# Performance work log

Hardware: AMD Instinct MI355X
Metric: run time of the kernel (lower is better)

The kernel has to match this reference:

```python
import jax, jax.numpy as jnp
import numpy as np


def setup_inputs() -> dict:
    key = jax.random.key(0)
    ks = jax.random.split(key, 5)
    B, S, C = 512, 512, 96
    emissions = jax.random.normal(ks[0], (B, S, C), dtype=jnp.float32)
    tags = jax.random.randint(ks[1], (B, S), 0, C, dtype=jnp.int64)
    masks = jnp.ones((B, S), dtype=bool)
    start_transitions = jax.random.uniform(ks[2], (C,), jnp.float32, -0.1, 0.1)
    end_transitions = jax.random.uniform(ks[3], (C,), jnp.float32, -0.1, 0.1)
    transitions = jax.random.uniform(ks[4], (C, C), jnp.float32, -0.1, 0.1)
    return {
        "emissions": emissions,
        "tags": tags,
        "masks": masks,
        "start_transitions": start_transitions,
        "end_transitions": end_transitions,
        "transitions": transitions,
    }


def _crf_llh(emissions, tags, masks, start_transitions, end_transitions, transitions):
    # to time-major: (S, B, C), (S, B)
    emissions = jnp.swapaxes(emissions, 0, 1)
    tags = jnp.swapaxes(tags, 0, 1)
    masks = jnp.swapaxes(masks, 0, 1)
    S, B, C = emissions.shape
    maskf = masks.astype(emissions.dtype)

    # ---- numerator: score of the gold tag path (fully vectorized over time) ----
    em_scores = jnp.take_along_axis(emissions, tags[:, :, None], axis=2)[:, :, 0]  # (S, B)
    trans_scores = transitions[tags[:-1], tags[1:]]  # (S-1, B)
    score = start_transitions[tags[0]] + em_scores[0]
    score = score + jnp.sum((trans_scores + em_scores[1:]) * maskf[1:], axis=0)
    seq_ends = masks.astype(jnp.int32).sum(axis=0) - 1  # (B,)
    last_tags = tags[seq_ends, jnp.arange(B)]
    numerator = score + end_transitions[last_tags]

    # ---- denominator: forward algorithm (sequential logsumexp recurrence) ----
    alpha0 = start_transitions[None, :] + emissions[0]  # (B, C)

    def step(alpha, inp):
        em_i, m_i = inp  # (B, C), (B,)
        # (B, C_prev, C_next)
        scores = alpha[:, :, None] + transitions[None, :, :] + em_i[:, None, :]
        next_alpha = jax.scipy.special.logsumexp(scores, axis=1)
        alpha = jnp.where(m_i[:, None], next_alpha, alpha)
        return alpha, None

    alpha, _ = jax.lax.scan(step, alpha0, (emissions[1:], masks[1:]))
    denominator = jax.scipy.special.logsumexp(alpha + end_transitions[None, :], axis=1)

    return jnp.mean(numerator - denominator)


def reference(emissions, tags, masks, start_transitions, end_transitions, transitions):
    return _crf_llh(emissions, tags, masks, start_transitions, end_transitions, transitions)
```

## Files before the change

### kernel.cpp

```cpp
#include <hip/hip_runtime.h>
#include <hip/hip_bf16.h>
#include <math.h>


#define BATCH 512
#define SEQ   512
#define NC    96
#define NTHR  64
#define NEG_INF (-1e30f)
#define SC    0.25f
#define LSC   1.3862943611198906f

typedef __fp16 half2v __attribute__((ext_vector_type(2)));

#define DPP_STEP_F(v, op, ctrl)                                              \
    v = op(v, __int_as_float(__builtin_amdgcn_update_dpp(                    \
            __float_as_int(v), __float_as_int(v), (ctrl), 0xf, 0xf, false)))

__device__ __forceinline__ float wave_max_all(float v) {
    DPP_STEP_F(v, fmaxf, 0x111);
    DPP_STEP_F(v, fmaxf, 0x112);
    DPP_STEP_F(v, fmaxf, 0x114);
    DPP_STEP_F(v, fmaxf, 0x118);
    DPP_STEP_F(v, fmaxf, 0x142);
    DPP_STEP_F(v, fmaxf, 0x143);
    return __int_as_float(__builtin_amdgcn_readlane(__float_as_int(v), 63));
}
__device__ __forceinline__ float fadd_(float a, float b) { return a + b; }
__device__ __forceinline__ float wave_sum_all(float v) {
    DPP_STEP_F(v, fadd_, 0x111);
    DPP_STEP_F(v, fadd_, 0x112);
    DPP_STEP_F(v, fadd_, 0x114);
    DPP_STEP_F(v, fadd_, 0x118);
    DPP_STEP_F(v, fadd_, 0x142);
    DPP_STEP_F(v, fadd_, 0x143);
    return __int_as_float(__builtin_amdgcn_readlane(__float_as_int(v), 63));
}

__global__ __launch_bounds__(NTHR, 1)
void crf_llh_kernel(const float* __restrict__ em,
                    const int*   __restrict__ tags,
                    const int*   __restrict__ masks,
                    const float* __restrict__ startT,
                    const float* __restrict__ endT,
                    const float* __restrict__ trans,
                    float*       __restrict__ out)
{
    const int b = blockIdx.x;
    const int l = threadIdx.x;
    const bool active = (l < 48);
    const int j0 = active ? 2 * l     : 0;
    const int j1 = active ? 2 * l + 1 : 0;

    __shared__ __align__(16) half2v qsh[48];

    const float* em_b    = em    + (size_t)b * SEQ * NC;
    const int*   tags_b  = tags  + b * SEQ;
    const int*   masks_b = masks + b * SEQ;

    half2v e0[48], e1[48];
    #pragma unroll
    for (int k = 0; k < 48; ++k) {
        const float t00 = trans[(2 * k)     * NC + j0];
        const float t01 = trans[(2 * k + 1) * NC + j0];
        const float t10 = trans[(2 * k)     * NC + j1];
        const float t11 = trans[(2 * k + 1) * NC + j1];
        e0[k] = __builtin_amdgcn_cvt_pkrtz(__expf(t00), __expf(t01));
        e1[k] = __builtin_amdgcn_cvt_pkrtz(__expf(t10), __expf(t11));
    }

    float a0 = active ? (startT[j0] + em_b[j0]) : NEG_INF;
    float a1 = active ? (startT[j1] + em_b[j1]) : NEG_INF;
    float m  = wave_max_all(fmaxf(a0, a1));

    const float2* em2 = reinterpret_cast<const float2*>(em_b);
    float2 emA = em2[1 * (NC / 2) + l % 48];
    float2 emB = em2[2 * (NC / 2) + l % 48];
    int mkA = masks_b[1];
    int mkB = masks_b[2];

    for (int s = 1; s < SEQ; ++s) {
        const int sp = (s + 2 < SEQ) ? (s + 2) : (SEQ - 1);
        const float2 emN = em2[sp * (NC / 2) + l % 48];
        const int    mkN = masks_b[sp];

        const float wm = wave_max_all(fmaxf(a0, a1));

        const float p0 = __expf(a0 - m) * SC;
        const float p1 = __expf(a1 - m) * SC;
        const half2v ph = __builtin_amdgcn_cvt_pkrtz(p0, p1);
        if (active) qsh[l] = ph;
        __syncthreads();

        float acc0a = 0.f, acc0b = 0.f, acc1a = 0.f, acc1b = 0.f;
        const uint4* q4 = reinterpret_cast<const uint4*>(qsh);
        #pragma unroll
        for (int t = 0; t < 12; ++t) {
            const uint4 qv = q4[t];
            const half2v qx = __builtin_bit_cast(half2v, qv.x);
            const half2v qy = __builtin_bit_cast(half2v, qv.y);
            const half2v qz = __builtin_bit_cast(half2v, qv.z);
            const half2v qw = __builtin_bit_cast(half2v, qv.w);
            acc0a = __builtin_amdgcn_fdot2(qx, e0[4 * t + 0], acc0a, false);
            acc1a = __builtin_amdgcn_fdot2(qx, e1[4 * t + 0], acc1a, false);
            acc0a = __builtin_amdgcn_fdot2(qy, e0[4 * t + 1], acc0a, false);
            acc1a = __builtin_amdgcn_fdot2(qy, e1[4 * t + 1], acc1a, false);
            acc0b = __builtin_amdgcn_fdot2(qz, e0[4 * t + 2], acc0b, false);
            acc1b = __builtin_amdgcn_fdot2(qz, e1[4 * t + 2], acc1b, false);
            acc0b = __builtin_amdgcn_fdot2(qw, e0[4 * t + 3], acc0b, false);
            acc1b = __builtin_amdgcn_fdot2(qw, e1[4 * t + 3], acc1b, false);
        }
        const float acc0 = acc0a + acc0b;
        const float acc1 = acc1a + acc1b;

        const bool upd = active && (mkA != 0);
        const float na0 = m + __logf(acc0) + LSC + emA.x;
        const float na1 = m + __logf(acc1) + LSC + emA.y;
        a0 = upd ? na0 : a0;
        a1 = upd ? na1 : a1;
        m = wm;

        emA = emB; emB = emN;
        mkA = mkB; mkB = mkN;
    }

    const float v0 = active ? (a0 + endT[j0]) : NEG_INF;
    const float v1 = active ? (a1 + endT[j1]) : NEG_INF;
    const float M  = wave_max_all(fmaxf(v0, v1));
    const float e  = active ? (__expf(v0 - M) + __expf(v1 - M)) : 0.f;
    const float denom = M + __logf(wave_sum_all(e));

    float nsum = 0.f;
    float msum = 0.f;
    #pragma unroll
    for (int k = 0; k < SEQ / NTHR; ++k) {
        const int s  = l + NTHR * k;
        const int tg = tags_b[s];
        const int mk = masks_b[s];
        msum += (mk ? 1.f : 0.f);
        if (s == 0) {
            nsum += startT[tg] + em_b[tg];
        } else if (mk) {
            nsum += trans[tags_b[s - 1] * NC + tg] + em_b[s * NC + tg];
        }
    }
    nsum = wave_sum_all(nsum);
    msum = wave_sum_all(msum);
    if (l == 0) {
        const int cnt  = (int)msum;
        const int last = tags_b[cnt - 1];
        atomicAdd(out, (nsum + endT[last] - denom) * (1.0f / (float)BATCH));
    }
}

extern "C" void kernel_launch(void* const* d_in, const int* in_sizes, int n_in,
                              void* d_out, int out_size, void* d_ws, size_t ws_size,
                              hipStream_t stream) {
    const float* em     = (const float*)d_in[0];
    const int*   tags   = (const int*)  d_in[1];
    const int*   masks  = (const int*)  d_in[2];
    const float* startT = (const float*)d_in[3];
    const float* endT   = (const float*)d_in[4];
    const float* trans  = (const float*)d_in[5];
    float* out = (float*)d_out;

    (void)hipMemsetAsync(out, 0, sizeof(float), stream);
    crf_llh_kernel<<<BATCH, NTHR, 0, stream>>>(em, tags, masks, startT, endT, trans, out);
}
```

Baseline: 420.6 us.

## Batch 16 sequences per wave and compute forward recurrence with MFMA

The kernel now handles 16 batch rows per single-wave block and computes each step's 16x96 by 96x96 product of exp(alpha) and exp(transitions) with fp16 MFMA instead of per-lane dot products. Each row is rescaled by a power of two taken from its max exponent, and the exponents are accumulated in an integer, so no logs are needed inside the loop. The aim is to replace scalar fdot2 work and one block per sequence with matrix-core throughput. The cost is only 32 blocks on a large GPU, LDS round-trips each step, and added fp16 rounding error.

```diff
diff --git a/kernel.cpp b/kernel.cpp
--- a/kernel.cpp
+++ b/kernel.cpp
@@ -6,26 +6,20 @@
 #define BATCH 512
 #define SEQ   512
 #define NC    96
-#define NTHR  64
-#define NEG_INF (-1e30f)
-#define SC    0.25f
-#define LSC   1.3862943611198906f
+#define CH    16
+#define NBLK  (BATCH / CH)
+#define PAD   104
+#define LN2   0.69314718055994531f
+#define LN2X4 2.7725887222397812f
 
 typedef __fp16 half2v __attribute__((ext_vector_type(2)));
+typedef __fp16 half8v __attribute__((ext_vector_type(8)));
+typedef float  f32x4  __attribute__((ext_vector_type(4)));
 
 #define DPP_STEP_F(v, op, ctrl)                                              \
     v = op(v, __int_as_float(__builtin_amdgcn_update_dpp(                    \
             __float_as_int(v), __float_as_int(v), (ctrl), 0xf, 0xf, false)))
 
-__device__ __forceinline__ float wave_max_all(float v) {
-    DPP_STEP_F(v, fmaxf, 0x111);
-    DPP_STEP_F(v, fmaxf, 0x112);
-    DPP_STEP_F(v, fmaxf, 0x114);
-    DPP_STEP_F(v, fmaxf, 0x118);
-    DPP_STEP_F(v, fmaxf, 0x142);
-    DPP_STEP_F(v, fmaxf, 0x143);
-    return __int_as_float(__builtin_amdgcn_readlane(__float_as_int(v), 63));
-}
 __device__ __forceinline__ float fadd_(float a, float b) { return a + b; }
 __device__ __forceinline__ float wave_sum_all(float v) {
     DPP_STEP_F(v, fadd_, 0x111);
@@ -36,8 +30,15 @@
     DPP_STEP_F(v, fadd_, 0x143);
     return __int_as_float(__builtin_amdgcn_readlane(__float_as_int(v), 63));
 }
-
-__global__ __launch_bounds__(NTHR, 1)
+__device__ __forceinline__ float bperm_f(int lanesrc, float v) {
+    return __int_as_float(__builtin_amdgcn_ds_bpermute(
+        (lanesrc & 63) << 2, __float_as_int(v)));
+}
+__device__ __forceinline__ int bperm_i(int lanesrc, int v) {
+    return __builtin_amdgcn_ds_bpermute((lanesrc & 63) << 2, v);
+}
+
+__global__ __launch_bounds__(64, 1)
 void crf_llh_kernel(const float* __restrict__ em,
                     const int*   __restrict__ tags,
                     const int*   __restrict__ masks,
@@ -48,109 +49,188 @@
 {
     const int b = blockIdx.x;
     const int l = threadIdx.x;
-    const bool active = (l < 48);
-    const int j0 = active ? 2 * l     : 0;
-    const int j1 = active ? 2 * l + 1 : 0;
-
-    __shared__ __align__(16) half2v qsh[48];
-
-    const float* em_b    = em    + (size_t)b * SEQ * NC;
-    const int*   tags_b  = tags  + b * SEQ;
-    const int*   masks_b = masks + b * SEQ;
-
-    half2v e0[48], e1[48];
-    #pragma unroll
-    for (int k = 0; k < 48; ++k) {
-        const float t00 = trans[(2 * k)     * NC + j0];
-        const float t01 = trans[(2 * k + 1) * NC + j0];
-        const float t10 = trans[(2 * k)     * NC + j1];
-        const float t11 = trans[(2 * k + 1) * NC + j1];
-        e0[k] = __builtin_amdgcn_cvt_pkrtz(__expf(t00), __expf(t01));
-        e1[k] = __builtin_amdgcn_cvt_pkrtz(__expf(t10), __expf(t11));
-    }
-
-    float a0 = active ? (startT[j0] + em_b[j0]) : NEG_INF;
-    float a1 = active ? (startT[j1] + em_b[j1]) : NEG_INF;
-    float m  = wave_max_all(fmaxf(a0, a1));
-
-    const float2* em2 = reinterpret_cast<const float2*>(em_b);
-    float2 emA = em2[1 * (NC / 2) + l % 48];
-    float2 emB = em2[2 * (NC / 2) + l % 48];
-    int mkA = masks_b[1];
-    int mkB = masks_b[2];
+    const int c = l & 15;
+    const int q = l >> 4;
+
+    __shared__ __fp16 wl[CH * PAD];
+    __shared__ float  maxsh[CH];
+
+    half8v Bf[3][6];
+    #pragma unroll
+    for (int kt = 0; kt < 3; ++kt) {
+        #pragma unroll
+        for (int nt = 0; nt < 6; ++nt) {
+            #pragma unroll
+            for (int jp = 0; jp < 4; ++jp) {
+                const int k0 = 32 * kt + 8 * q + 2 * jp;
+                const int n  = 16 * nt + c;
+                const half2v pe = __builtin_amdgcn_cvt_pkrtz(
+                    __expf(trans[(k0)     * NC + n]),
+                    __expf(trans[(k0 + 1) * NC + n]));
+                Bf[kt][nt][2 * jp]     = pe[0];
+                Bf[kt][nt][2 * jp + 1] = pe[1];
+            }
+        }
+    }
+
+    const size_t gc = (size_t)(b * CH + c);
+    const float* em_c = em + gc * SEQ * NC;
+    const int*   mk_c = masks + gc * SEQ;
+    const int*   tg_c = tags  + gc * SEQ;
+
+    half8v Af[3];
+    float M0;
+    int   S;
+    {
+        float a0[24];
+        float mx = -1e30f;
+        #pragma unroll
+        for (int kt = 0; kt < 3; ++kt)
+            #pragma unroll
+            for (int j = 0; j < 8; ++j) {
+                const int k = 32 * kt + 8 * q + j;
+                const float v = startT[k] + em_c[k];
+                a0[kt * 8 + j] = v;
+                mx = fmaxf(mx, v);
+            }
+        mx = fmaxf(mx, bperm_f(l ^ 16, mx));
+        mx = fmaxf(mx, bperm_f(l ^ 32, mx));
+        M0 = mx;
+        S  = 1;
+        #pragma unroll
+        for (int kt = 0; kt < 3; ++kt)
+            #pragma unroll
+            for (int j = 0; j < 8; ++j)
+                Af[kt][j] = (__fp16)(__expf(a0[kt * 8 + j] - M0) * 0.5f);
+    }
+
+    size_t emb[4];
+    #pragma unroll
+    for (int r = 0; r < 4; ++r)
+        emb[r] = (size_t)(b * CH + 4 * q + r) * SEQ * NC + c;
+
+    float emA[24], emB[24];
+    #pragma unroll
+    for (int nt = 0; nt < 6; ++nt)
+        #pragma unroll
+        for (int r = 0; r < 4; ++r) {
+            emA[nt * 4 + r] = em[emb[r] + (size_t)1 * NC + 16 * nt];
+            emB[nt * 4 + r] = em[emb[r] + (size_t)2 * NC + 16 * nt];
+        }
+    int mkA = mk_c[1], mkB = mk_c[2];
 
     for (int s = 1; s < SEQ; ++s) {
         const int sp = (s + 2 < SEQ) ? (s + 2) : (SEQ - 1);
-        const float2 emN = em2[sp * (NC / 2) + l % 48];
-        const int    mkN = masks_b[sp];
-
-        const float wm = wave_max_all(fmaxf(a0, a1));
-
-        const float p0 = __expf(a0 - m) * SC;
-        const float p1 = __expf(a1 - m) * SC;
-        const half2v ph = __builtin_amdgcn_cvt_pkrtz(p0, p1);
-        if (active) qsh[l] = ph;
-        __syncthreads();
-
-        float acc0a = 0.f, acc0b = 0.f, acc1a = 0.f, acc1b = 0.f;
-        const uint4* q4 = reinterpret_cast<const uint4*>(qsh);
-        #pragma unroll
-        for (int t = 0; t < 12; ++t) {
-            const uint4 qv = q4[t];
-            const half2v qx = __builtin_bit_cast(half2v, qv.x);
-            const half2v qy = __builtin_bit_cast(half2v, qv.y);
-            const half2v qz = __builtin_bit_cast(half2v, qv.z);
-            const half2v qw = __builtin_bit_cast(half2v, qv.w);
-            acc0a = __builtin_amdgcn_fdot2(qx, e0[4 * t + 0], acc0a, false);
-            acc1a = __builtin_amdgcn_fdot2(qx, e1[4 * t + 0], acc1a, false);
-            acc0a = __builtin_amdgcn_fdot2(qy, e0[4 * t + 1], acc0a, false);
-            acc1a = __builtin_amdgcn_fdot2(qy, e1[4 * t + 1], acc1a, false);
-            acc0b = __builtin_amdgcn_fdot2(qz, e0[4 * t + 2], acc0b, false);
-            acc1b = __builtin_amdgcn_fdot2(qz, e1[4 * t + 2], acc1b, false);
-            acc0b = __builtin_amdgcn_fdot2(qw, e0[4 * t + 3], acc0b, false);
-            acc1b = __builtin_amdgcn_fdot2(qw, e1[4 * t + 3], acc1b, false);
-        }
-        const float acc0 = acc0a + acc0b;
-        const float acc1 = acc1a + acc1b;
-
-        const bool upd = active && (mkA != 0);
-        const float na0 = m + __logf(acc0) + LSC + emA.x;
-        const float na1 = m + __logf(acc1) + LSC + emA.y;
-        a0 = upd ? na0 : a0;
-        a1 = upd ? na1 : a1;
-        m = wm;
-
-        emA = emB; emB = emN;
+        float emN[24];
+        #pragma unroll
+        for (int nt = 0; nt < 6; ++nt)
+            #pragma unroll
+            for (int r = 0; r < 4; ++r)
+                emN[nt * 4 + r] = em[emb[r] + (size_t)sp * NC + 16 * nt];
+        const int mkN = mk_c[sp];
+
+        float Fv[24];
+        #pragma unroll
+        for (int i = 0; i < 24; ++i) Fv[i] = __expf(emA[i] - LN2X4);
+
+        float mr[4] = {-1e30f, -1e30f, -1e30f, -1e30f};
+        #pragma unroll
+        for (int nt = 0; nt < 6; ++nt) {
+            f32x4 a = {0.f, 0.f, 0.f, 0.f};
+            a = __builtin_amdgcn_mfma_f32_16x16x32_f16(Af[0], Bf[0][nt], a, 0, 0, 0);
+            a = __builtin_amdgcn_mfma_f32_16x16x32_f16(Af[1], Bf[1][nt], a, 0, 0, 0);
+            a = __builtin_amdgcn_mfma_f32_16x16x32_f16(Af[2], Bf[2][nt], a, 0, 0, 0);
+            #pragma unroll
+            for (int r = 0; r < 4; ++r) {
+                const float wv = a[r] * Fv[nt * 4 + r];
+                mr[r] = fmaxf(mr[r], wv);
+                wl[(4 * q + r) * PAD + 16 * nt + c] = (__fp16)wv;
+            }
+        }
+
+        #pragma unroll
+        for (int r = 0; r < 4; ++r) {
+            float v = mr[r];
+            DPP_STEP_F(v, fmaxf, 0x111);
+            DPP_STEP_F(v, fmaxf, 0x112);
+            DPP_STEP_F(v, fmaxf, 0x114);
+            DPP_STEP_F(v, fmaxf, 0x118);
+            if (c == 15) maxsh[4 * q + r] = v;
+        }
+
+        const float mxc = maxsh[c];
+        half8v A0 = *(const half8v*)&wl[c * PAD + 0  + q * 8];
+        half8v A1 = *(const half8v*)&wl[c * PAD + 32 + q * 8];
+        half8v A2 = *(const half8v*)&wl[c * PAD + 64 + q * 8];
+
+        const int eb = (int)((__float_as_uint(mxc) >> 23) & 255u) - 126;
+        unsigned hbits = ((unsigned)(15 - eb)) << 10;
+        hbits |= hbits << 16;
+        const half2v sc2 = __builtin_bit_cast(half2v, hbits);
+
+        half8v An[3] = {A0, A1, A2};
+        #pragma unroll
+        for (int kt = 0; kt < 3; ++kt) {
+            #pragma unroll
+            for (int jp = 0; jp < 4; ++jp) {
+                half2v t = {An[kt][2 * jp], An[kt][2 * jp + 1]};
+                t = t * sc2;
+                An[kt][2 * jp]     = t[0];
+                An[kt][2 * jp + 1] = t[1];
+            }
+        }
+        if (mkA) {
+            Af[0] = An[0]; Af[1] = An[1]; Af[2] = An[2];
+            S += eb + 4;
+        }
+
+        #pragma unroll
+        for (int i = 0; i < 24; ++i) { emA[i] = emB[i]; emB[i] = emN[i]; }
         mkA = mkB; mkB = mkN;
     }
 
-    const float v0 = active ? (a0 + endT[j0]) : NEG_INF;
-    const float v1 = active ? (a1 + endT[j1]) : NEG_INF;
-    const float M  = wave_max_all(fmaxf(v0, v1));
-    const float e  = active ? (__expf(v0 - M) + __expf(v1 - M)) : 0.f;
-    const float denom = M + __logf(wave_sum_all(e));
+    float dsum = 0.f;
+    #pragma unroll
+    for (int kt = 0; kt < 3; ++kt)
+        #pragma unroll
+        for (int j = 0; j < 8; ++j) {
+            const int k = 32 * kt + 8 * q + j;
+            dsum += (float)Af[kt][j] * __expf(endT[k]);
+        }
+    dsum += bperm_f(l ^ 16, dsum);
+    dsum += bperm_f(l ^ 32, dsum);
+    const float denom = M0 + (float)S * LN2 + __logf(dsum);
 
     float nsum = 0.f;
-    float msum = 0.f;
-    #pragma unroll
-    for (int k = 0; k < SEQ / NTHR; ++k) {
-        const int s  = l + NTHR * k;
-        const int tg = tags_b[s];
-        const int mk = masks_b[s];
-        msum += (mk ? 1.f : 0.f);
-        if (s == 0) {
-            nsum += startT[tg] + em_b[tg];
-        } else if (mk) {
-            nsum += trans[tags_b[s - 1] * NC + tg] + em_b[s * NC + tg];
-        }
-    }
-    nsum = wave_sum_all(nsum);
-    msum = wave_sum_all(msum);
-    if (l == 0) {
-        const int cnt  = (int)msum;
-        const int last = tags_b[cnt - 1];
-        atomicAdd(out, (nsum + endT[last] - denom) * (1.0f / (float)BATCH));
-    }
+    int   cnt  = 0;
+    {
+        const int s0 = q * 128;
+        int tprev = (s0 > 0) ? tg_c[s0 - 1] : 0;
+        for (int i = 0; i < 128; ++i) {
+            const int s  = s0 + i;
+            const int tg = tg_c[s];
+            const int mk = mk_c[s];
+            cnt += mk ? 1 : 0;
+            if (s == 0) {
+                nsum += startT[tg] + em_c[tg];
+            } else if (mk) {
+                nsum += trans[tprev * NC + tg] + em_c[(size_t)s * NC + tg];
+            }
+            tprev = tg;
+        }
+    }
+    nsum += bperm_f(l ^ 16, nsum);
+    nsum += bperm_f(l ^ 32, nsum);
+    cnt  += bperm_i(l ^ 16, cnt);
+    cnt  += bperm_i(l ^ 32, cnt);
+
+    float llh = 0.f;
+    if (q == 0) {
+        const int last = tg_c[cnt - 1];
+        llh = (nsum + endT[last]) - denom;
+    }
+    const float tot = wave_sum_all(llh);
+    if (l == 0) atomicAdd(out, tot * (1.0f / (float)BATCH));
 }
 
 extern "C" void kernel_launch(void* const* d_in, const int* in_sizes, int n_in,
@@ -165,5 +245,5 @@
     float* out = (float*)d_out;
 
     (void)hipMemsetAsync(out, 0, sizeof(float), stream);
-    crf_llh_kernel<<<BATCH, NTHR, 0, stream>>>(em, tags, masks, startT, endT, trans, out);
-}
+    crf_llh_kernel<<<NBLK, 64, 0, stream>>>(em, tags, masks, startT, endT, trans, out);
+}
```

Measured after the change: 729.6 us. 1.73x slower.
